# Kernel optimization log

Measured on AMD Instinct MI355X. Metric: run time of the kernel, lower is better.

The kernel has to match this reference:

```python
import jax, jax.numpy as jnp
import numpy as np

VOCAB = 131072
EMB_DIM = 2048
N_PAD = 2048  # next power of two >= EMB_DIM
CB = 65536    # 2^16 codebook entries of E8 (8-dim) vectors


def fht(x):
    """Unnormalized fast Hadamard transform over the last dim (power of 2)."""
    n = x.shape[-1]
    orig = x.shape
    x = x.reshape(-1, n)
    h = 1
    while h < n:
        x = x.reshape(-1, n // (2 * h), 2, h)
        a, b = x[:, :, 0, :], x[:, :, 1, :]
        x = jnp.stack([a + b, a - b], axis=2).reshape(-1, n)
        h *= 2
    return x.reshape(orig)


def setup_inputs() -> dict:
    key = jax.random.key(0)
    k = jax.random.split(key, 6)
    input_ids = jax.random.randint(k[0], (8, 2048), 0, VOCAB, dtype=jnp.int32)
    Qidxs = jax.random.randint(k[1], (VOCAB, N_PAD // 8), -32768, 32768, dtype=jnp.int32).astype(jnp.int16)
    Qidxs2 = jax.random.randint(k[2], (VOCAB, N_PAD // 8), -32768, 32768, dtype=jnp.int32).astype(jnp.int16)
    codebook = (jax.random.normal(k[3], (CB, 8), dtype=jnp.float32) * 0.5).astype(jnp.float16)
    codebook2 = (jax.random.normal(k[4], (CB, 8), dtype=jnp.float32) * 0.5).astype(jnp.float16)
    SV = (jax.random.uniform(k[5], (N_PAD,), dtype=jnp.float32) * 0.5 + 0.75).astype(jnp.float16)
    Wscale = jnp.asarray(0.02, dtype=jnp.float32)
    inv_resid_scale = jnp.asarray(0.3, dtype=jnp.float32)
    return {"input_ids": input_ids, "Qidxs": Qidxs, "Qidxs2": Qidxs2,
            "codebook": codebook, "codebook2": codebook2, "SV": SV,
            "Wscale": Wscale, "inv_resid_scale": inv_resid_scale}


def reference(input_ids, Qidxs, Qidxs2, codebook, codebook2, SV, Wscale, inv_resid_scale):
    flat = input_ids.reshape(-1)                 # [N]
    n_tok = flat.shape[0]
    # stage 1: row gather -> packed int16 -> codebook gather
    rows1 = Qidxs[flat]                          # [N, N_PAD//8] int16
    idx1 = (rows1.astype(jnp.int32) & 0xFFFF).reshape(-1)
    deq = codebook[idx1].reshape(n_tok, N_PAD).astype(jnp.float32)
    # stage 2 residual
    rows2 = Qidxs2[flat]
    idx2 = (rows2.astype(jnp.int32) & 0xFFFF).reshape(-1)
    deq2 = codebook2[idx2].reshape(n_tok, N_PAD).astype(jnp.float32)
    deq = deq + deq2 * inv_resid_scale
    deq = deq * Wscale
    deq = fht(deq)
    deq = deq * SV.astype(jnp.float32)
    out = deq[:, :EMB_DIM].astype(jnp.float16)   # out dtype = SV.dtype
    return out.reshape(input_ids.shape + (EMB_DIM,))
```

## Files before the change

kernel.cpp:

```cpp
#include <hip/hip_runtime.h>
#include <hip/hip_fp16.h>

typedef int   v4i __attribute__((ext_vector_type(4)));
typedef unsigned int v4u __attribute__((ext_vector_type(4)));

constexpr int TPW        = 4;
constexpr int NTOK_BLK   = 32;
constexpr int SLICE_ROWS = 4096;
constexpr int NPASS      = 16;

__global__ __launch_bounds__(256) void cvt_kernel(
    const float* __restrict__ cb1, const float* __restrict__ cb2,
    unsigned int* __restrict__ o1, unsigned int* __restrict__ o2)
{
    const int r = blockIdx.x * 256 + threadIdx.x;
    const float* src = (r < 65536) ? (cb1 + (size_t)r * 8)
                                   : (cb2 + (size_t)(r - 65536) * 8);
    unsigned int* dst = (r < 65536) ? (o1 + (size_t)r * 4)
                                    : (o2 + (size_t)(r - 65536) * 4);
    const float4 a = ((const float4*)src)[0];
    const float4 b = ((const float4*)src)[1];
    __half2 h0 = __floats2half2_rn(a.x, a.y);
    __half2 h1 = __floats2half2_rn(a.z, a.w);
    __half2 h2 = __floats2half2_rn(b.x, b.y);
    __half2 h3 = __floats2half2_rn(b.z, b.w);
    v4u o;
    o.x = *(unsigned int*)&h0; o.y = *(unsigned int*)&h1;
    o.z = *(unsigned int*)&h2; o.w = *(unsigned int*)&h3;
    *(v4u*)dst = o;
}

__device__ __forceinline__ void convert8(const v4u g1[4], const v4u g2[4],
    const float ws, const float ws2, float v[32])
{
    #pragma unroll
    for (int c = 0; c < 4; ++c) {
        const unsigned int au[4] = { g1[c].x, g1[c].y, g1[c].z, g1[c].w };
        const unsigned int bu[4] = { g2[c].x, g2[c].y, g2[c].z, g2[c].w };
        #pragma unroll
        for (int p = 0; p < 4; ++p) {
            const float2 fa = __half22float2(*(const __half2*)&au[p]);
            const float2 fb = __half22float2(*(const __half2*)&bu[p]);
            v[8*c + 2*p]     = fa.x * ws + fb.x * ws2;
            v[8*c + 2*p + 1] = fa.y * ws + fb.y * ws2;
        }
    }
}

__device__ __forceinline__ void process_tok(float v[32], float* __restrict__ L,
    const int lane, const float* __restrict__ SV, float* __restrict__ outp)
{
    #pragma unroll
    for (int h = 1; h < 32; h <<= 1) {
        #pragma unroll
        for (int r = 0; r < 32; ++r) {
            if ((r & h) == 0) { float a = v[r], b = v[r + h]; v[r] = a + b; v[r + h] = a - b; }
        }
    }

    __builtin_amdgcn_wave_barrier();
    {
        const int t4 = lane >> 2, tl = lane & 3;
        #pragma unroll
        for (int j = 0; j < 32; ++j) {
            const int col = (((t4 ^ (j & 15)) << 2) | tl);
            L[(j << 6) + col] = v[j];
        }
    }
    __builtin_amdgcn_wave_barrier();

    const int j0 = lane >> 1;
    const int b  = lane & 1;
    float w[32];
    {
        const float4* Lr = (const float4*)(L + (j0 << 6));
        #pragma unroll
        for (int c = 0; c < 8; ++c) {
            const int ch = ((b << 3) + c) ^ (j0 & 15);
            const float4 f = Lr[ch];
            w[4*c + 0] = f.x; w[4*c + 1] = f.y; w[4*c + 2] = f.z; w[4*c + 3] = f.w;
        }
    }
    __builtin_amdgcn_wave_barrier();

    const int ebase = (b << 10) | j0;
    float svv[32];
    #pragma unroll
    for (int r = 0; r < 32; ++r) svv[r] = SV[ebase + (r << 5)];

    #pragma unroll
    for (int h = 1; h < 32; h <<= 1) {
        #pragma unroll
        for (int r = 0; r < 32; ++r) {
            if ((r & h) == 0) { float a = w[r], bb = w[r + h]; w[r] = a + bb; w[r + h] = a - bb; }
        }
    }

    #pragma unroll
    for (int r = 0; r < 32; ++r) {
        const float o = __shfl_xor(w[r], 1, 64);
        w[r] = b ? (o - w[r]) : (w[r] + o);
    }

    #pragma unroll
    for (int r = 0; r < 32; ++r) {
        const int e = ebase + (r << 5);
        __builtin_nontemporal_store(w[r] * svv[r], &outp[e]);
    }
}

__global__ __launch_bounds__(512, 2) void e8rht_kernel_h(
    const int* __restrict__ input_ids,
    const int* __restrict__ Qidxs,
    const int* __restrict__ Qidxs2,
    const unsigned int* __restrict__ cb1h,
    const unsigned int* __restrict__ cb2h,
    const float* __restrict__ SV,
    const float* __restrict__ Wscale,
    const float* __restrict__ inv_resid,
    float* __restrict__ out)
{
    __shared__ __align__(16) unsigned int slice[SLICE_ROWS * 4];
    const int wave = threadIdx.x >> 6;
    const int lane = threadIdx.x & 63;

    const float ws  = Wscale[0];
    const float ws2 = ws * inv_resid[0];
    const int tok0 = blockIdx.x * NTOK_BLK + wave * TPW;

    int i1[TPW][4], i2[TPW][4];
    #pragma unroll
    for (int t = 0; t < TPW; ++t) {
        const int tid = input_ids[tok0 + t];
        const v4i a = __builtin_nontemporal_load((const v4i*)(Qidxs  + (size_t)tid * 256 + lane * 4));
        const v4i b = __builtin_nontemporal_load((const v4i*)(Qidxs2 + (size_t)tid * 256 + lane * 4));
        i1[t][0] = a.x & 0xFFFF; i1[t][1] = a.y & 0xFFFF;
        i1[t][2] = a.z & 0xFFFF; i1[t][3] = a.w & 0xFFFF;
        i2[t][0] = b.x & 0xFFFF; i2[t][1] = b.y & 0xFFFF;
        i2[t][2] = b.z & 0xFFFF; i2[t][3] = b.w & 0xFFFF;
    }

    v4u g1[TPW][4], g2[TPW][4];

    const int soff = wave * 2048 + lane * 4;
    v4u st[8];
    {
        const unsigned int* s = cb1h + soff;
        #pragma unroll
        for (int k = 0; k < 8; ++k) st[k] = *(const v4u*)(s + k * 256);
    }

    #pragma unroll 1
    for (int p = 0; p < 2 * NPASS; ++p) {
        __syncthreads();
        unsigned int* dst = slice + soff;
        #pragma unroll
        for (int k = 0; k < 8; ++k) *(v4u*)(dst + k * 256) = st[k];
        if (p + 1 < 2 * NPASS) {
            const int pn = p + 1;
            const unsigned int* s = (pn < NPASS
                ? cb1h + (size_t)pn * (SLICE_ROWS * 4)
                : cb2h + (size_t)(pn - NPASS) * (SLICE_ROWS * 4)) + soff;
            #pragma unroll
            for (int k = 0; k < 8; ++k) st[k] = *(const v4u*)(s + k * 256);
        }
        __syncthreads();
        if (p < NPASS) {
            #pragma unroll
            for (int t = 0; t < TPW; ++t) {
                #pragma unroll
                for (int c = 0; c < 4; ++c) {
                    if ((i1[t][c] >> 12) == p)
                        g1[t][c] = *(const v4u*)(slice + (size_t)(i1[t][c] & (SLICE_ROWS - 1)) * 4);
                }
            }
        } else {
            #pragma unroll
            for (int t = 0; t < TPW; ++t) {
                #pragma unroll
                for (int c = 0; c < 4; ++c) {
                    if ((i2[t][c] >> 12) == p - NPASS)
                        g2[t][c] = *(const v4u*)(slice + (size_t)(i2[t][c] & (SLICE_ROWS - 1)) * 4);
                }
            }
        }
    }
    __syncthreads();

    float* L = ((float*)slice) + wave * 2048;
    #pragma unroll
    for (int t = 0; t < TPW; ++t) {
        float v[32];
        convert8(g1[t], g2[t], ws, ws2, v);
        process_tok(v, L, lane, SV, out + (size_t)(tok0 + t) * 2048);
    }
}

__global__ __launch_bounds__(256, 4) void e8rht_kernel_f(
    const int* __restrict__ input_ids,
    const int* __restrict__ Qidxs,
    const int* __restrict__ Qidxs2,
    const float* __restrict__ codebook,
    const float* __restrict__ codebook2,
    const float* __restrict__ SV,
    const float* __restrict__ Wscale,
    const float* __restrict__ inv_resid,
    float* __restrict__ out)
{
    __shared__ __align__(16) float lds[4 * 2048];
    const int wave = threadIdx.x >> 6;
    const int lane = threadIdx.x & 63;
    const int tok  = blockIdx.x * 4 + wave;

    const float ws  = Wscale[0];
    const float ws2 = ws * inv_resid[0];
    const int tid = input_ids[tok];

    const int4 q1 = *(const int4*)(Qidxs  + (size_t)tid * 256 + lane * 4);
    const int4 q2 = *(const int4*)(Qidxs2 + (size_t)tid * 256 + lane * 4);

    float v[32];
    {
        const int i1[4] = { q1.x & 0xFFFF, q1.y & 0xFFFF, q1.z & 0xFFFF, q1.w & 0xFFFF };
        const int i2[4] = { q2.x & 0xFFFF, q2.y & 0xFFFF, q2.z & 0xFFFF, q2.w & 0xFFFF };
        #pragma unroll
        for (int c = 0; c < 4; ++c) {
            const float4* r1 = (const float4*)(codebook  + (size_t)i1[c] * 8);
            const float4* r2 = (const float4*)(codebook2 + (size_t)i2[c] * 8);
            const float4 a0 = r1[0], a1 = r1[1];
            const float4 b0 = r2[0], b1 = r2[1];
            v[8*c+0]=a0.x*ws+b0.x*ws2; v[8*c+1]=a0.y*ws+b0.y*ws2;
            v[8*c+2]=a0.z*ws+b0.z*ws2; v[8*c+3]=a0.w*ws+b0.w*ws2;
            v[8*c+4]=a1.x*ws+b1.x*ws2; v[8*c+5]=a1.y*ws+b1.y*ws2;
            v[8*c+6]=a1.z*ws+b1.z*ws2; v[8*c+7]=a1.w*ws+b1.w*ws2;
        }
    }
    #pragma unroll
    for (int h = 1; h < 32; h <<= 1)
        #pragma unroll
        for (int r = 0; r < 32; ++r)
            if ((r & h) == 0) { float a=v[r],b=v[r+h]; v[r]=a+b; v[r+h]=a-b; }

    float* L = lds + wave * 2048;
    {
        const int t4 = lane >> 2, tl = lane & 3;
        #pragma unroll
        for (int j = 0; j < 32; ++j)
            L[(j << 6) + (((t4 ^ (j & 15)) << 2) | tl)] = v[j];
    }
    __syncthreads();
    const int j0 = lane >> 1;
    const int b  = lane & 1;
    float w[32];
    {
        const float4* Lr = (const float4*)(L + (j0 << 6));
        #pragma unroll
        for (int c = 0; c < 8; ++c) {
            const float4 f = Lr[((b << 3) + c) ^ (j0 & 15)];
            w[4*c+0]=f.x; w[4*c+1]=f.y; w[4*c+2]=f.z; w[4*c+3]=f.w;
        }
    }
    #pragma unroll
    for (int h = 1; h < 32; h <<= 1)
        #pragma unroll
        for (int r = 0; r < 32; ++r)
            if ((r & h) == 0) { float a=w[r],bb=w[r+h]; w[r]=a+bb; w[r+h]=a-bb; }
    #pragma unroll
    for (int r = 0; r < 32; ++r) {
        const float o = __shfl_xor(w[r], 1, 64);
        w[r] = b ? (o - w[r]) : (w[r] + o);
    }
    const size_t obase = (size_t)tok * 2048;
    const int ebase = (b << 10) | j0;
    #pragma unroll
    for (int r = 0; r < 32; ++r) {
        const int e = ebase + (r << 5);
        out[obase + e] = w[r] * SV[e];
    }
}

extern "C" void kernel_launch(void* const* d_in, const int* in_sizes, int n_in,
                              void* d_out, int out_size, void* d_ws, size_t ws_size,
                              hipStream_t stream) {
    const int* input_ids   = (const int*)d_in[0];
    const int* Qidxs       = (const int*)d_in[1];
    const int* Qidxs2      = (const int*)d_in[2];
    const float* codebook  = (const float*)d_in[3];
    const float* codebook2 = (const float*)d_in[4];
    const float* SV        = (const float*)d_in[5];
    const float* wscale    = (const float*)d_in[6];
    const float* irs       = (const float*)d_in[7];
    float* out             = (float*)d_out;

    const int n_tok = in_sizes[0];

    const size_t cb_h_bytes = (size_t)65536 * 8 * 2;
    if (ws_size >= 2 * cb_h_bytes && (n_tok % NTOK_BLK) == 0) {
        unsigned int* cb1h = (unsigned int*)d_ws;
        unsigned int* cb2h = (unsigned int*)((char*)d_ws + cb_h_bytes);
        cvt_kernel<<<512, 256, 0, stream>>>(codebook, codebook2, cb1h, cb2h);
        const int grid = n_tok / NTOK_BLK;
        e8rht_kernel_h<<<grid, 512, 0, stream>>>(input_ids, Qidxs, Qidxs2,
                                                 cb1h, cb2h, SV, wscale, irs, out);
    } else {
        const int grid = n_tok / 4;
        e8rht_kernel_f<<<grid, 256, 0, stream>>>(input_ids, Qidxs, Qidxs2,
                                                 codebook, codebook2, SV,
                                                 wscale, irs, out);
    }
}
```

Before: 392.1 us.

## Double-buffer codebook slices in LDS using direct global-to-LDS loads

Replaces the register-staged codebook slice copy with global_load_lds direct transfers into a double-buffered LDS region, so the next slice streams into LDS while the current one is gathered from. Manual vmcnt/lgkmcnt waits and raw s_barriers with sched_barriers replace __syncthreads. LDS use doubles to 128KB per block and launch bounds drop to one block per CU, which cuts occupancy in exchange for fewer register staging instructions and better overlap.

```diff
diff --git a/kernel.cpp b/kernel.cpp
--- a/kernel.cpp
+++ b/kernel.cpp
@@ -8,6 +8,7 @@
 constexpr int NTOK_BLK   = 32;
 constexpr int SLICE_ROWS = 4096;
 constexpr int NPASS      = 16;
+constexpr int NPASS_ALL  = 32;
 
 __global__ __launch_bounds__(256) void cvt_kernel(
     const float* __restrict__ cb1, const float* __restrict__ cb2,
@@ -30,6 +31,13 @@
     *(v4u*)dst = o;
 }
 
+__device__ __forceinline__ void gload_lds16(const unsigned int* g, unsigned int* l)
+{
+    __builtin_amdgcn_global_load_lds(
+        (const __attribute__((address_space(1))) unsigned int*)g,
+        (__attribute__((address_space(3))) unsigned int*)l, 16, 0, 0);
+}
+
 __device__ __forceinline__ void convert8(const v4u g1[4], const v4u g2[4],
     const float ws, const float ws2, float v[32])
 {
@@ -109,7 +117,7 @@
     }
 }
 
-__global__ __launch_bounds__(512, 2) void e8rht_kernel_h(
+__global__ __launch_bounds__(512, 1) void e8rht_kernel_h(
     const int* __restrict__ input_ids,
     const int* __restrict__ Qidxs,
     const int* __restrict__ Qidxs2,
@@ -120,7 +128,7 @@
     const float* __restrict__ inv_resid,
     float* __restrict__ out)
 {
-    __shared__ __align__(16) unsigned int slice[SLICE_ROWS * 4];
+    __shared__ __align__(16) unsigned int slice[2][SLICE_ROWS * 4];
     const int wave = threadIdx.x >> 6;
     const int lane = threadIdx.x & 63;
 
@@ -143,51 +151,60 @@
     v4u g1[TPW][4], g2[TPW][4];
 
     const int soff = wave * 2048 + lane * 4;
-    v4u st[8];
+
     {
         const unsigned int* s = cb1h + soff;
-        #pragma unroll
-        for (int k = 0; k < 8; ++k) st[k] = *(const v4u*)(s + k * 256);
+        unsigned int* d = &slice[0][wave * 2048];
+        #pragma unroll
+        for (int k = 0; k < 8; ++k) gload_lds16(s + k * 256, d + k * 256);
     }
 
     #pragma unroll 1
-    for (int p = 0; p < 2 * NPASS; ++p) {
-        __syncthreads();
-        unsigned int* dst = slice + soff;
-        #pragma unroll
-        for (int k = 0; k < 8; ++k) *(v4u*)(dst + k * 256) = st[k];
-        if (p + 1 < 2 * NPASS) {
+    for (int p = 0; p < NPASS_ALL; ++p) {
+        unsigned int* buf = &slice[p & 1][0];
+        if (p < NPASS_ALL - 1) {
             const int pn = p + 1;
             const unsigned int* s = (pn < NPASS
                 ? cb1h + (size_t)pn * (SLICE_ROWS * 4)
                 : cb2h + (size_t)(pn - NPASS) * (SLICE_ROWS * 4)) + soff;
+            unsigned int* d = &slice[pn & 1][wave * 2048];
             #pragma unroll
-            for (int k = 0; k < 8; ++k) st[k] = *(const v4u*)(s + k * 256);
-        }
-        __syncthreads();
+            for (int k = 0; k < 8; ++k) gload_lds16(s + k * 256, d + k * 256);
+            asm volatile("s_waitcnt vmcnt(8)" ::: "memory");
+        } else {
+            asm volatile("s_waitcnt vmcnt(0)" ::: "memory");
+        }
+        __builtin_amdgcn_sched_barrier(0);
+        __builtin_amdgcn_s_barrier();
+        __builtin_amdgcn_sched_barrier(0);
+
         if (p < NPASS) {
             #pragma unroll
             for (int t = 0; t < TPW; ++t) {
                 #pragma unroll
                 for (int c = 0; c < 4; ++c) {
                     if ((i1[t][c] >> 12) == p)
-                        g1[t][c] = *(const v4u*)(slice + (size_t)(i1[t][c] & (SLICE_ROWS - 1)) * 4);
+                        g1[t][c] = *(const v4u*)(buf + (size_t)(i1[t][c] & (SLICE_ROWS - 1)) * 4);
                 }
             }
         } else {
+            const int ps = p - NPASS;
             #pragma unroll
             for (int t = 0; t < TPW; ++t) {
                 #pragma unroll
                 for (int c = 0; c < 4; ++c) {
-                    if ((i2[t][c] >> 12) == p - NPASS)
-                        g2[t][c] = *(const v4u*)(slice + (size_t)(i2[t][c] & (SLICE_ROWS - 1)) * 4);
+                    if ((i2[t][c] >> 12) == ps)
+                        g2[t][c] = *(const v4u*)(buf + (size_t)(i2[t][c] & (SLICE_ROWS - 1)) * 4);
                 }
             }
         }
-    }
-    __syncthreads();
-
-    float* L = ((float*)slice) + wave * 2048;
+        asm volatile("s_waitcnt lgkmcnt(0)" ::: "memory");
+        __builtin_amdgcn_sched_barrier(0);
+        __builtin_amdgcn_s_barrier();
+        __builtin_amdgcn_sched_barrier(0);
+    }
+
+    float* L = ((float*)&slice[0][0]) + wave * 2048;
     #pragma unroll
     for (int t = 0; t < TPW; ++t) {
         float v[32];
```

Result: faster. 347.5 us (-11.4%).
